# Kernel tuning notes

Measured on AMD Instinct MI355X. Metric: run time of the kernel, lower is better.

The kernel has to match this reference:

```python
import jax, jax.numpy as jnp
import numpy as np

B, T = 64, 512
L, D = 2048, 512


def setup_inputs() -> dict:
    key = jax.random.key(0)
    k1, k2, k3 = jax.random.split(key, 3)
    label_sequences = jax.random.randint(k1, (B, T), 0, L)
    source_embeddings = jax.random.normal(k2, (L, D), dtype=jnp.float32)
    target_embeddings = jax.random.normal(k3, (L, D), dtype=jnp.float32)
    return {
        "label_sequences": label_sequences,
        "source_embeddings": source_embeddings,
        "target_embeddings": target_embeddings,
    }


def reference(label_sequences, source_embeddings, target_embeddings):
    # source_index = labels[:, :-1], target_index = labels[:, 1:]
    src_idx = label_sequences[:, :-1]          # [B, T-1]
    tgt_idx = label_sequences[:, 1:]           # [B, T-1]
    # Gather source embeddings per transition pair: [B, T-1, D]
    src = source_embeddings[src_idx]
    # Logits over all target labels: [B, T-1, L]
    logits = jnp.einsum("btd,ld->btl", src, target_embeddings)
    # Row-wise log_softmax over target labels (dim=1 in torch == last axis here)
    logp = jax.nn.log_softmax(logits, axis=-1)
    # Pick the actual next label's log-probability: [B, T-1]
    scores = jnp.take_along_axis(logp, tgt_idx[..., None], axis=-1)[..., 0]
    return scores
```

## Files before the change

kernel.cpp:

```cpp
#include <hip/hip_runtime.h>
#include <hip/hip_bf16.h>

#define L_CLS 2048
#define D_DIM 512
#define T_SZ  512
#define NT    511
#define NOUT  (64 * NT)
#define NCHUNK 16
#define LOG2E 1.4426950408889634f
#define LN2   0.6931471805599453f
#define SHIFT 128.0f

typedef __attribute__((ext_vector_type(8))) short bf16x8;
typedef __attribute__((ext_vector_type(4))) float f32x4;

static __device__ __forceinline__ short f2bf(float x) {
    return (short)__bfloat16_as_ushort(__float2bfloat16(x));
}
static __device__ __forceinline__ float bits2f(unsigned short u) {
    union { unsigned int i; float f; } v; v.i = ((unsigned int)u) << 16; return v.f;
}

__global__ void conv_bf16(const float* __restrict__ srcE, const float* __restrict__ tgtE,
                          __hip_bfloat16* __restrict__ Sb, __hip_bfloat16* __restrict__ Tb) {
    int i = blockIdx.x * blockDim.x + threadIdx.x;
    if (i >= (L_CLS * D_DIM) / 8) return;
    const f32x4* s4 = reinterpret_cast<const f32x4*>(srcE) + i * 2;
    const f32x4* t4 = reinterpret_cast<const f32x4*>(tgtE) + i * 2;
    f32x4 s0 = s4[0], s1 = s4[1];
    f32x4 t0 = t4[0], t1 = t4[1];
    bf16x8 so, to;
#pragma unroll
    for (int j = 0; j < 4; ++j) {
        so[j] = f2bf(s0[j]); so[j + 4] = f2bf(s1[j]);
        to[j] = f2bf(t0[j]); to[j + 4] = f2bf(t1[j]);
    }
    reinterpret_cast<bf16x8*>(Sb)[i] = so;
    reinterpret_cast<bf16x8*>(Tb)[i] = to;
}

__launch_bounds__(512)
__global__ void gemm_lse_bf16(const __hip_bfloat16* __restrict__ Sb,
                              const __hip_bfloat16* __restrict__ Tb,
                              float* __restrict__ psum) {
    __shared__ __hip_bfloat16 Blds[128 * 128];

    const int tid  = threadIdx.x;
    const int wave = tid >> 6;
    const int lane = tid & 63;
    const int lr   = lane & 15;
    const int hi   = lane >> 4;
    const int C    = blockIdx.x * 128;
    const int R    = blockIdx.y * 128 + wave * 16;

    f32x4 acc[8];
#pragma unroll
    for (int ct = 0; ct < 8; ++ct) acc[ct] = (f32x4){0.f, 0.f, 0.f, 0.f};

    bf16x8 stg[4], an[4];
#pragma unroll
    for (int i = 0; i < 4; ++i) {
        int p = tid + 512 * i;
        stg[i] = *reinterpret_cast<const bf16x8*>(
            &Tb[(C + (p >> 4)) * D_DIM + (p & 15) * 8]);
    }
#pragma unroll
    for (int ks = 0; ks < 4; ++ks)
        an[ks] = *reinterpret_cast<const bf16x8*>(
            &Sb[(R + lr) * D_DIM + ks * 32 + hi * 8]);

#pragma unroll 1
    for (int s = 0; s < 4; ++s) {
#pragma unroll
        for (int i = 0; i < 4; ++i) {
            int p   = tid + 512 * i;
            int row = p >> 4;
            int e   = (p & 15) * 8;
            *reinterpret_cast<bf16x8*>(
                &Blds[row * 128 + (e ^ ((row & 7) << 3))]) = stg[i];
        }
        bf16x8 a[4];
#pragma unroll
        for (int ks = 0; ks < 4; ++ks) a[ks] = an[ks];
        __syncthreads();

        if (s < 3) {
#pragma unroll
            for (int i = 0; i < 4; ++i) {
                int p = tid + 512 * i;
                stg[i] = *reinterpret_cast<const bf16x8*>(
                    &Tb[(C + (p >> 4)) * D_DIM + (s + 1) * 128 + (p & 15) * 8]);
            }
#pragma unroll
            for (int ks = 0; ks < 4; ++ks)
                an[ks] = *reinterpret_cast<const bf16x8*>(
                    &Sb[(R + lr) * D_DIM + (s + 1) * 128 + ks * 32 + hi * 8]);
        }

#pragma unroll
        for (int ks = 0; ks < 4; ++ks) {
#pragma unroll
            for (int ct = 0; ct < 8; ++ct) {
                int row = ct * 16 + lr;
                int e   = (ks * 32 + hi * 8) ^ ((lr & 7) << 3);
                bf16x8 b = *reinterpret_cast<const bf16x8*>(&Blds[row * 128 + e]);
                acc[ct] = __builtin_amdgcn_mfma_f32_16x16x32_bf16(a[ks], b, acc[ct], 0, 0, 0);
            }
        }
        __syncthreads();
    }

    float p[4];
#pragma unroll
    for (int i = 0; i < 4; ++i) {
        p[i] = 0.f;
#pragma unroll
        for (int ct = 0; ct < 8; ++ct)
            p[i] += exp2f(acc[ct][i] * LOG2E - SHIFT);
    }
#pragma unroll
    for (int off = 1; off < 16; off <<= 1)
#pragma unroll
        for (int i = 0; i < 4; ++i) p[i] += __shfl_xor(p[i], off);
    if (lr == 0) {
#pragma unroll
        for (int i = 0; i < 4; ++i)
            psum[(R + hi * 4 + i) * NCHUNK + blockIdx.x] = p[i];
    }
}

__launch_bounds__(256)
__global__ void scores_dot(const int* __restrict__ labels,
                           const __hip_bfloat16* __restrict__ Sb,
                           const __hip_bfloat16* __restrict__ Tb,
                           const float* __restrict__ psum,
                           float* __restrict__ out) {
    const int wid  = blockIdx.x * 4 + (threadIdx.x >> 6);
    const int lane = threadIdx.x & 63;
    const int b = wid / NT;
    const int t = wid - b * NT;
    const int src = labels[b * T_SZ + t];
    const int tgt = labels[b * T_SZ + t + 1];

    bf16x8 sv = *reinterpret_cast<const bf16x8*>(&Sb[src * D_DIM + lane * 8]);
    bf16x8 tv = *reinterpret_cast<const bf16x8*>(&Tb[tgt * D_DIM + lane * 8]);
    float acc = 0.f;
#pragma unroll
    for (int j = 0; j < 8; ++j)
        acc += bits2f((unsigned short)sv[j]) * bits2f((unsigned short)tv[j]);

    float ps = (lane < NCHUNK) ? psum[src * NCHUNK + lane] : 0.f;
#pragma unroll
    for (int off = 32; off; off >>= 1) {
        acc += __shfl_xor(acc, off);
        ps  += __shfl_xor(ps, off);
    }
    if (lane == 0) out[wid] = acc - (log2f(ps) + SHIFT) * LN2;
}

extern "C" void kernel_launch(void* const* d_in, const int* in_sizes, int n_in,
                              void* d_out, int out_size, void* d_ws, size_t ws_size,
                              hipStream_t stream) {
    const int*   labels = (const int*)d_in[0];
    const float* srcE   = (const float*)d_in[1];
    const float* tgtE   = (const float*)d_in[2];
    float*       out    = (float*)d_out;

    const size_t tbl = (size_t)L_CLS * D_DIM;
    __hip_bfloat16* Sb = (__hip_bfloat16*)d_ws;
    __hip_bfloat16* Tb = Sb + tbl;
    float* psum = (float*)((char*)d_ws + 2 * tbl * sizeof(__hip_bfloat16));

    conv_bf16<<<(int)(tbl / 8 + 255) / 256, 256, 0, stream>>>(srcE, tgtE, Sb, Tb);
    gemm_lse_bf16<<<dim3(NCHUNK, 16), 512, 0, stream>>>(Sb, Tb, psum);
    scores_dot<<<NOUT / 4, 256, 0, stream>>>(labels, Sb, Tb, psum, out);
}
```

Measured before the change: 30.38 us.

## Fuse target-logit dot products into GEMM epilogue, add light combine kernel

Moves the per-position gathered source·target dot products into the tail of the GEMM/logsumexp kernel: each of the 256 workgroups handles 128 outputs, one wave per 16, two at a time. A small elementwise combine kernel then reads psum with vector loads and the stored logits to produce the scores. The aim is to shrink the final kernel and overlap the gather work with GEMM blocks that would otherwise be idle. The cost is a longer GEMM kernel tail, extra workspace traffic for the logits, and the gathers are spread over only 256 workgroups.

```diff
diff --git a/kernel.cpp b/kernel.cpp
--- a/kernel.cpp
+++ b/kernel.cpp
@@ -40,9 +40,11 @@
 }
 
 __launch_bounds__(512)
-__global__ void gemm_lse_bf16(const __hip_bfloat16* __restrict__ Sb,
+__global__ void gemm_lse_bf16(const int* __restrict__ labels,
+                              const __hip_bfloat16* __restrict__ Sb,
                               const __hip_bfloat16* __restrict__ Tb,
-                              float* __restrict__ psum) {
+                              float* __restrict__ psum,
+                              float* __restrict__ logits) {
     __shared__ __hip_bfloat16 Blds[128 * 128];
 
     const int tid  = threadIdx.x;
@@ -127,35 +129,58 @@
         for (int i = 0; i < 4; ++i)
             psum[(R + hi * 4 + i) * NCHUNK + blockIdx.x] = p[i];
     }
+
+    const int wgid = blockIdx.y * NCHUNK + blockIdx.x;
+    const int obase = wgid * 128 + wave * 16;
+#pragma unroll 1
+    for (int q = 0; q < 16; q += 2) {
+        int o0 = obase + q, o1 = obase + q + 1;
+        float d0 = 0.f, d1 = 0.f;
+        bool v0 = o0 < NOUT, v1 = o1 < NOUT;
+        if (v0) {
+            int b = o0 / NT, t = o0 - b * NT;
+            int src = labels[b * T_SZ + t], tgt = labels[b * T_SZ + t + 1];
+            bf16x8 svv = *reinterpret_cast<const bf16x8*>(&Sb[src * D_DIM + lane * 8]);
+            bf16x8 tvv = *reinterpret_cast<const bf16x8*>(&Tb[tgt * D_DIM + lane * 8]);
+#pragma unroll
+            for (int j = 0; j < 8; ++j)
+                d0 += bits2f((unsigned short)svv[j]) * bits2f((unsigned short)tvv[j]);
+        }
+        if (v1) {
+            int b = o1 / NT, t = o1 - b * NT;
+            int src = labels[b * T_SZ + t], tgt = labels[b * T_SZ + t + 1];
+            bf16x8 svv = *reinterpret_cast<const bf16x8*>(&Sb[src * D_DIM + lane * 8]);
+            bf16x8 tvv = *reinterpret_cast<const bf16x8*>(&Tb[tgt * D_DIM + lane * 8]);
+#pragma unroll
+            for (int j = 0; j < 8; ++j)
+                d1 += bits2f((unsigned short)svv[j]) * bits2f((unsigned short)tvv[j]);
+        }
+#pragma unroll
+        for (int off = 32; off; off >>= 1) {
+            d0 += __shfl_xor(d0, off);
+            d1 += __shfl_xor(d1, off);
+        }
+        if (lane == 0 && v0) logits[o0] = d0;
+        if (lane == 0 && v1) logits[o1] = d1;
+    }
 }
 
 __launch_bounds__(256)
-__global__ void scores_dot(const int* __restrict__ labels,
-                           const __hip_bfloat16* __restrict__ Sb,
-                           const __hip_bfloat16* __restrict__ Tb,
-                           const float* __restrict__ psum,
-                           float* __restrict__ out) {
-    const int wid  = blockIdx.x * 4 + (threadIdx.x >> 6);
-    const int lane = threadIdx.x & 63;
-    const int b = wid / NT;
-    const int t = wid - b * NT;
-    const int src = labels[b * T_SZ + t];
-    const int tgt = labels[b * T_SZ + t + 1];
-
-    bf16x8 sv = *reinterpret_cast<const bf16x8*>(&Sb[src * D_DIM + lane * 8]);
-    bf16x8 tv = *reinterpret_cast<const bf16x8*>(&Tb[tgt * D_DIM + lane * 8]);
-    float acc = 0.f;
-#pragma unroll
-    for (int j = 0; j < 8; ++j)
-        acc += bits2f((unsigned short)sv[j]) * bits2f((unsigned short)tv[j]);
-
-    float ps = (lane < NCHUNK) ? psum[src * NCHUNK + lane] : 0.f;
-#pragma unroll
-    for (int off = 32; off; off >>= 1) {
-        acc += __shfl_xor(acc, off);
-        ps  += __shfl_xor(ps, off);
-    }
-    if (lane == 0) out[wid] = acc - (log2f(ps) + SHIFT) * LN2;
+__global__ void combine(const int* __restrict__ labels,
+                        const float* __restrict__ psum,
+                        const float* __restrict__ logits,
+                        float* __restrict__ out) {
+    int o = blockIdx.x * 256 + threadIdx.x;
+    if (o >= NOUT) return;
+    int b = o / NT;
+    int t = o - b * NT;
+    int src = labels[b * T_SZ + t];
+
+    const f32x4* pv = reinterpret_cast<const f32x4*>(psum + src * NCHUNK);
+    f32x4 s0 = pv[0], s1 = pv[1], s2 = pv[2], s3 = pv[3];
+    float S = (s0[0]+s0[1]+s0[2]+s0[3]) + (s1[0]+s1[1]+s1[2]+s1[3])
+            + (s2[0]+s2[1]+s2[2]+s2[3]) + (s3[0]+s3[1]+s3[2]+s3[3]);
+    out[o] = logits[o] - (log2f(S) + SHIFT) * LN2;
 }
 
 extern "C" void kernel_launch(void* const* d_in, const int* in_sizes, int n_in,
@@ -169,9 +194,10 @@
     const size_t tbl = (size_t)L_CLS * D_DIM;
     __hip_bfloat16* Sb = (__hip_bfloat16*)d_ws;
     __hip_bfloat16* Tb = Sb + tbl;
-    float* psum = (float*)((char*)d_ws + 2 * tbl * sizeof(__hip_bfloat16));
+    float* psum   = (float*)((char*)d_ws + 2 * tbl * sizeof(__hip_bfloat16));
+    float* logits = psum + (size_t)L_CLS * NCHUNK;
 
     conv_bf16<<<(int)(tbl / 8 + 255) / 256, 256, 0, stream>>>(srcE, tgtE, Sb, Tb);
-    gemm_lse_bf16<<<dim3(NCHUNK, 16), 512, 0, stream>>>(Sb, Tb, psum);
-    scores_dot<<<NOUT / 4, 256, 0, stream>>>(labels, Sb, Tb, psum, out);
-}
+    gemm_lse_bf16<<<dim3(NCHUNK, 16), 512, 0, stream>>>(labels, Sb, Tb, psum, logits);
+    combine<<<(NOUT + 255) / 256, 256, 0, stream>>>(labels, psum, logits, out);
+}
```

New measurement: 36.69 us. +20.8%, slower.
